# Kernel tuning notes

Hardware: AMD Instinct MI355X
Metric: run time of the kernel (lower is better)

## Reference

```python
import jax, jax.numpy as jnp
import numpy as np

E, N, D, H = 500000, 100000, 8, 256
BN_EPS = 1e-5


def _batchnorm(x, gamma, beta):
    # BatchNorm1d in training mode: biased batch statistics over dim 0
    mu = jnp.mean(x, axis=0)
    var = jnp.var(x, axis=0)
    return (x - mu) * jax.lax.rsqrt(var + BN_EPS) * gamma + beta


def _encoder(x, W1, b1, gamma, beta, W2, b2):
    h = jax.nn.relu(x @ W1 + b1)
    h = _batchnorm(h, gamma, beta)
    return h @ W2 + b2


def setup_inputs() -> dict:
    key = jax.random.key(0)
    ks = jax.random.split(key, 24)
    s = 0.05  # weight init scale
    inp = {
        "edge_attr": jax.random.normal(ks[0], (E, D), dtype=jnp.float32),
        "node_features": jax.random.normal(ks[1], (N, D), dtype=jnp.float32),
        "edge_index": jax.random.randint(ks[2], (2, E), 0, N, dtype=jnp.int32),
        "e_W1": jax.random.normal(ks[3], (D, H)) * s,
        "e_b1": jax.random.normal(ks[4], (H,)) * s,
        "e_gamma": jnp.ones((H,), jnp.float32),
        "e_beta": jnp.zeros((H,), jnp.float32),
        "e_W2": jax.random.normal(ks[5], (H, H)) * s,
        "e_b2": jax.random.normal(ks[6], (H,)) * s,
        "n_W1": jax.random.normal(ks[7], (D, H)) * s,
        "n_b1": jax.random.normal(ks[8], (H,)) * s,
        "n_gamma": jnp.ones((H,), jnp.float32),
        "n_beta": jnp.zeros((H,), jnp.float32),
        "n_W2": jax.random.normal(ks[9], (H, H)) * s,
        "n_b2": jax.random.normal(ks[10], (H,)) * s,
        "Wv": jax.random.normal(ks[11], (H, H)) * s,
        "bv": jax.random.normal(ks[12], (H,)) * s,
        "Wo": jax.random.normal(ks[13], (H, H)) * s,
        "bo": jax.random.normal(ks[14], (H,)) * s,
        "Wp": jax.random.normal(ks[15], (H, D)) * s,
        "bp": jax.random.normal(ks[16], (D,)) * s,
    }
    return inp


def reference(edge_attr, node_features, edge_index,
              e_W1, e_b1, e_gamma, e_beta, e_W2, e_b2,
              n_W1, n_b1, n_gamma, n_beta, n_W2, n_b2,
              Wv, bv, Wo, bo, Wp, bp):
    # edge encoder: Linear -> ReLU -> BatchNorm1d -> Linear
    edge_encoded = _encoder(edge_attr, e_W1, e_b1, e_gamma, e_beta, e_W2, e_b2)

    # gather endpoint features and average (node dim == edge dim, slice is no-op)
    src = node_features[edge_index[0]]  # [E, D]
    tgt = node_features[edge_index[1]]  # [E, D]
    node_context = (src + tgt) * 0.5
    node_encoded = _encoder(node_context, n_W1, n_b1, n_gamma, n_beta, n_W2, n_b2)

    # MultiheadAttention with seq_len=1: softmax over one key is exactly 1,
    # so output = out_proj(v_proj(node_encoded)); q/k projections cancel.
    attn_out = (node_encoded @ Wv + bv) @ Wo + bo  # [E, H]

    edge_attr_enhanced = attn_out @ Wp + bp  # [E, D]
    return edge_attr + 0.5 * edge_attr_enhanced
```

## Files before the change

kernel.cpp:

```cpp
#include <hip/hip_runtime.h>
#include <hip/hip_bf16.h>
#include <string.h>

#define E_CNT 500000
#define N_CNT 100000
#define HID   256
#define NTILE 31250

typedef short short8 __attribute__((ext_vector_type(8)));
typedef float f32x4 __attribute__((ext_vector_type(4)));

__device__ __forceinline__ unsigned short f2bf(float f){
  union { float f; unsigned int i; } v; v.f = f;
  unsigned int u = v.i;
  u = u + 0x7FFFu + ((u >> 16) & 1u);
  return (unsigned short)(u >> 16);
}

__device__ __forceinline__ unsigned int pk_bf16(float a, float b){
  __hip_bfloat162 p = __float22bfloat162_rn(make_float2(a, b));
  unsigned int u; memcpy(&u, &p, 4); return u;
}

__device__ __forceinline__ void init_w1_lds(unsigned short* w1l,
                                            const float* W1, const float* b1,
                                            int tid){
  int ch = tid;
  #pragma unroll
  for (int j = 0; j < 8; ++j){
    unsigned short w = f2bf(W1[j * HID + ch]);
    w1l[ch * 24 + j]     = w;
    w1l[ch * 24 + 8 + j] = w;
  }
  w1l[ch * 24 + 16] = f2bf(2.0f * b1[ch]);
  #pragma unroll
  for (int j = 17; j < 24; ++j) w1l[ch * 24 + j] = 0;
  if (tid < 32) w1l[256 * 24 + tid] = 0;
}

__global__ __launch_bounds__(256, 3) void k1_stats(
    const int* __restrict__ eidx, const float* __restrict__ nf,
    const float* __restrict__ W1, const float* __restrict__ b1,
    float* __restrict__ part, float* __restrict__ bd2)
{
  __shared__ unsigned short w1l[256 * 24 + 32];
  __shared__ unsigned short ctx[4][16 * 40];
  __shared__ float sred[2][4][128];

  const int tid = threadIdx.x, lane = tid & 63, wid = tid >> 6;
  const int cg = wid & 1;
  const int pair = (blockIdx.x * 4 + wid) >> 1;
  const int npair = gridDim.x * 2;
  const int m = lane & 15, q = lane >> 4;
  const int r = lane >> 2, side = (lane >> 1) & 1, half = lane & 1;

  if (blockIdx.x == 0 && tid < 16) bd2[tid] = 0.f;

  init_w1_lds(w1l, W1, b1, tid);

  unsigned short* myctx = ctx[wid];
  for (int i = lane; i < 16 * 40; i += 64) myctx[i] = 0;
  if (lane < 16) myctx[lane * 40 + 16] = 0x3F80;
  __syncthreads();

  short8 w1fr[8];
  #pragma unroll
  for (int nt = 0; nt < 8; ++nt)
    w1fr[nt] = *(const short8*)&w1l[((cg * 8 + nt) * 16 + m) * 24 + q * 8];

  const f32x4 z4 = {0.f, 0.f, 0.f, 0.f};
  f32x4 sacc[8], qacc[8];
  #pragma unroll
  for (int nt = 0; nt < 8; ++nt){ sacc[nt] = z4; qacc[nt] = z4; }

  int t = pair;
  float4 nfc = make_float4(0.f,0.f,0.f,0.f); int i1 = 0;
  if (t < NTILE){
    int id0 = eidx[side * E_CNT + t * 16 + r];
    nfc = ((const float4*)nf)[id0 * 2 + half];
  }
  { int tn = t + npair;
    if (tn < NTILE) i1 = eidx[side * E_CNT + tn * 16 + r]; }

  for (; t < NTILE; t += npair){
    *(uint2*)&myctx[r * 40 + side * 8 + half * 4] =
        make_uint2(pk_bf16(nfc.x, nfc.y), pk_bf16(nfc.z, nfc.w));

    int tn1 = t + npair, tn2 = t + 2 * npair;
    float4 nfn = make_float4(0.f,0.f,0.f,0.f); int i2 = 0;
    if (tn1 < NTILE) nfn = ((const float4*)nf)[i1 * 2 + half];
    if (tn2 < NTILE) i2 = eidx[side * E_CNT + tn2 * 16 + r];

    asm volatile("s_waitcnt lgkmcnt(0)" ::: "memory");
    short8 bfr = *(const short8*)&myctx[m * 40 + q * 8];
    #pragma unroll
    for (int nt = 0; nt < 8; ++nt){
      f32x4 c = __builtin_amdgcn_mfma_f32_16x16x32_bf16(w1fr[nt], bfr, z4, 0, 0, 0);
      f32x4 hv = __builtin_elementwise_max(c, z4);
      sacc[nt] += hv;
      qacc[nt] += hv * hv;
    }
    nfc = nfn; i1 = i2;
  }

  #pragma unroll
  for (int nt = 0; nt < 8; ++nt){
    #pragma unroll
    for (int i = 0; i < 4; ++i){
      float v = sacc[nt][i], w = qacc[nt][i];
      v += __shfl_xor(v, 1); w += __shfl_xor(w, 1);
      v += __shfl_xor(v, 2); w += __shfl_xor(w, 2);
      v += __shfl_xor(v, 4); w += __shfl_xor(w, 4);
      v += __shfl_xor(v, 8); w += __shfl_xor(w, 8);
      if (m == 0){
        int loc = nt * 16 + q * 4 + i;
        sred[0][wid][loc] = v;
        sred[1][wid][loc] = w;
      }
    }
  }
  __syncthreads();
  {
    int j = tid, hf = j >> 7, loc = j & 127;
    float s0 = sred[0][hf][loc] + sred[0][hf + 2][loc];
    float s1 = sred[1][hf][loc] + sred[1][hf + 2][loc];
    part[blockIdx.x * 512 + j]       = s0;
    part[blockIdx.x * 512 + 256 + j] = s1;
  }
}

__global__ __launch_bounds__(256) void kMid(
    const float* __restrict__ part, int nb,
    const float* __restrict__ gamma, const float* __restrict__ beta,
    const float* __restrict__ nW2,
    const float* __restrict__ Wv, const float* __restrict__ Wo,
    const float* __restrict__ Wp,
    const float* __restrict__ bv, const float* __restrict__ bo,
    const float* __restrict__ bp, const float* __restrict__ nb2,
    unsigned short* __restrict__ wd2t, float* __restrict__ bd2)
{
  __shared__ float WpL[2048];
  __shared__ float T1L[2048];
  __shared__ float T2L[2048];
  __shared__ float scr[2048];
  __shared__ float stL[8];
  const int t = threadIdx.x, b = blockIdx.x;

  for (int i = t; i < 2048; i += 256) WpL[i] = Wp[i];
  __syncthreads();

  {
    const float4* row = (const float4*)(Wo + t * HID);
    f32x4 a0 = {0.f,0.f,0.f,0.f}, a1 = {0.f,0.f,0.f,0.f};
    #pragma unroll 8
    for (int j4 = 0; j4 < 64; ++j4){
      float4 w = row[j4];
      const f32x4* xp = (const f32x4*)&WpL[j4 * 32];
      a0 += w.x * xp[0]; a1 += w.x * xp[1];
      a0 += w.y * xp[2]; a1 += w.y * xp[3];
      a0 += w.z * xp[4]; a1 += w.z * xp[5];
      a0 += w.w * xp[6]; a1 += w.w * xp[7];
    }
    *(f32x4*)&T1L[t * 8]     = a0;
    *(f32x4*)&T1L[t * 8 + 4] = a1;
  }
  __syncthreads();

  {
    const float4* row = (const float4*)(Wv + t * HID);
    f32x4 a0 = {0.f,0.f,0.f,0.f}, a1 = {0.f,0.f,0.f,0.f};
    #pragma unroll 8
    for (int j4 = 0; j4 < 64; ++j4){
      float4 w = row[j4];
      const f32x4* xp = (const f32x4*)&T1L[j4 * 32];
      a0 += w.x * xp[0]; a1 += w.x * xp[1];
      a0 += w.y * xp[2]; a1 += w.y * xp[3];
      a0 += w.z * xp[4]; a1 += w.z * xp[5];
      a0 += w.w * xp[6]; a1 += w.w * xp[7];
    }
    *(f32x4*)&T2L[t * 8]     = a0;
    *(f32x4*)&T2L[t * 8 + 4] = a1;
  }
  __syncthreads();

  {
    int cl = t >> 6, i = t & 63;
    int c = b * 4 + cl;
    float s0 = 0.f, s1 = 0.f;
    for (int b2 = i; b2 < nb; b2 += 64){
      s0 += part[b2 * 512 + c];
      s1 += part[b2 * 512 + 256 + c];
    }
    scr[cl * 128 + i]      = s0;
    scr[cl * 128 + 64 + i] = s1;
  }
  __syncthreads();
  if (t < 4){
    float s0 = 0.f, s1 = 0.f;
    for (int i = 0; i < 64; ++i){
      s0 += scr[t * 128 + i];
      s1 += scr[t * 128 + 64 + i];
    }
    const float invE = 1.0f / (float)E_CNT;
    float mu  = s0 * invE;
    float var = fmaxf(s1 * invE - mu * mu, 0.f);
    float s   = gamma[b * 4 + t] * rsqrtf(var + 4.0f * 1e-5f);
    stL[t]     = s;
    stL[4 + t] = beta[b * 4 + t] - mu * s;
  }
  __syncthreads();

  {
    int cl = t >> 6, d = (t >> 3) & 7, p8 = t & 7;
    int c = b * 4 + cl;
    const float* row = nW2 + c * HID;
    float a = 0.f;
    for (int j = p8 * 32; j < p8 * 32 + 32; ++j)
      a = fmaf(row[j], T2L[j * 8 + d], a);
    scr[t] = a;
  }
  __syncthreads();
  {
    int cl = t >> 6, d = (t >> 3) & 7, p8 = t & 7;
    if (p8 == 0){
      float w = 0.f;
      #pragma unroll
      for (int i = 0; i < 8; ++i) w += scr[t + i];
      int c = b * 4 + cl;
      wd2t[d * HID + c]       = f2bf(0.5f * stL[cl] * w);
      wd2t[(8 + d) * HID + c] = 0;
      scr[1024 + cl * 8 + d]  = stL[4 + cl] * w;
    }
  }
  __syncthreads();
  if (t < 8){
    float a = scr[1024 + t] + scr[1024 + 8 + t] +
              scr[1024 + 16 + t] + scr[1024 + 24 + t];
    #pragma unroll
    for (int jj = 0; jj < 4; ++jj){
      int j = 4 * b + jj;
      a = fmaf(nb2[j], T2L[j * 8 + t], a);
      a = fmaf(bv[j],  T1L[j * 8 + t], a);
      a = fmaf(bo[j],  WpL[j * 8 + t], a);
    }
    if (b == 0) a += bp[t];
    atomicAdd(&bd2[t], a);
  }
}

__global__ __launch_bounds__(256, 3) void k3_main(
    const int* __restrict__ eidx, const float* __restrict__ nf,
    const float* __restrict__ ea,
    const float* __restrict__ W1, const float* __restrict__ b1,
    const unsigned short* __restrict__ wd2t, const float* __restrict__ bd2,
    float* __restrict__ out)
{
  __shared__ unsigned short w1l[256 * 24 + 32];
  __shared__ unsigned short ctx[4][16 * 40];
  __shared__ unsigned short hbuf[4][16 * 264];

  const int tid = threadIdx.x, lane = tid & 63, wid = tid >> 6;
  const int gw = blockIdx.x * 4 + wid, ngw = gridDim.x * 4;
  const int m = lane & 15, q = lane >> 4;
  const int r = lane >> 2, side = (lane >> 1) & 1, half = lane & 1;

  init_w1_lds(w1l, W1, b1, tid);

  short8 w2fr[8];
  #pragma unroll
  for (int kb = 0; kb < 8; ++kb)
    w2fr[kb] = *(const short8*)&wd2t[m * HID + kb * 32 + q * 8];
  const float bd2v = (m < 8) ? 0.5f * bd2[m] : 0.f;

  unsigned short* myctx = ctx[wid];
  unsigned short* myh   = hbuf[wid];
  for (int i = lane; i < 16 * 40; i += 64) myctx[i] = 0;
  if (lane < 16) myctx[lane * 40 + 16] = 0x3F80;
  __syncthreads();

  short8 w1fr[16];
  #pragma unroll
  for (int nt = 0; nt < 16; ++nt)
    w1fr[nt] = *(const short8*)&w1l[(nt * 16 + m) * 24 + q * 8];

  const f32x4 z4 = {0.f, 0.f, 0.f, 0.f};

  int t = gw;
  float4 nfc = make_float4(0.f,0.f,0.f,0.f); int i1 = 0;
  if (t < NTILE){
    int id0 = eidx[side * E_CNT + t * 16 + r];
    nfc = ((const float4*)nf)[id0 * 2 + half];
  }
  { int tn = t + ngw;
    if (tn < NTILE) i1 = eidx[side * E_CNT + tn * 16 + r]; }

  const bool dok = (m < 8);
  for (; t < NTILE; t += ngw){
    *(uint2*)&myctx[r * 40 + side * 8 + half * 4] =
        make_uint2(pk_bf16(nfc.x, nfc.y), pk_bf16(nfc.z, nfc.w));

    float eav[4];
    #pragma unroll
    for (int i = 0; i < 4; ++i)
      eav[i] = dok ? ea[(t * 16 + q * 4 + i) * 8 + m] : 0.f;

    int tn1 = t + ngw, tn2 = t + 2 * ngw;
    float4 nfn = make_float4(0.f,0.f,0.f,0.f); int i2 = 0;
    if (tn1 < NTILE) nfn = ((const float4*)nf)[i1 * 2 + half];
    if (tn2 < NTILE) i2 = eidx[side * E_CNT + tn2 * 16 + r];

    asm volatile("s_waitcnt lgkmcnt(0)" ::: "memory");
    short8 bfr = *(const short8*)&myctx[m * 40 + q * 8];
    #pragma unroll
    for (int nt = 0; nt < 16; ++nt){
      f32x4 c = __builtin_amdgcn_mfma_f32_16x16x32_bf16(w1fr[nt], bfr, z4, 0, 0, 0);
      f32x4 hv = __builtin_elementwise_max(c, z4);
      *(uint2*)&myh[m * 264 + nt * 16 + q * 4] =
          make_uint2(pk_bf16(hv[0], hv[1]), pk_bf16(hv[2], hv[3]));
    }
    asm volatile("s_waitcnt lgkmcnt(0)" ::: "memory");
    f32x4 acc = z4;
    #pragma unroll
    for (int kb = 0; kb < 8; ++kb){
      short8 afr = *(const short8*)&myh[m * 264 + kb * 32 + q * 8];
      acc = __builtin_amdgcn_mfma_f32_16x16x32_bf16(afr, w2fr[kb], acc, 0, 0, 0);
    }
    if (dok){
      #pragma unroll
      for (int i = 0; i < 4; ++i){
        float o = eav[i] + acc[i] + bd2v;
        out[(t * 16 + q * 4 + i) * 8 + m] = o;
      }
    }
    nfc = nfn; i1 = i2;
  }
}

extern "C" void kernel_launch(void* const* d_in, const int* in_sizes, int n_in,
                              void* d_out, int out_size, void* d_ws, size_t ws_size,
                              hipStream_t stream)
{
  const float* ea   = (const float*)d_in[0];
  const float* nf   = (const float*)d_in[1];
  const int*   eidx = (const int*)d_in[2];
  const float* nW1    = (const float*)d_in[9];
  const float* nb1    = (const float*)d_in[10];
  const float* ngamma = (const float*)d_in[11];
  const float* nbeta  = (const float*)d_in[12];
  const float* nW2    = (const float*)d_in[13];
  const float* nb2    = (const float*)d_in[14];
  const float* Wv     = (const float*)d_in[15];
  const float* bv     = (const float*)d_in[16];
  const float* Wo     = (const float*)d_in[17];
  const float* bo     = (const float*)d_in[18];
  const float* Wp     = (const float*)d_in[19];
  const float* bp     = (const float*)d_in[20];

  long avail = (long)ws_size - 8192 - 64 - 16384;
  int nb = (int)(avail / 2048);
  if (nb > 768) nb = 768;
  if (nb < 1)   nb = 1;

  char* ws = (char*)d_ws;
  size_t off = (size_t)nb * 2048;
  float* ws_part          = (float*)(ws + 0);
  unsigned short* ws_wd2t = (unsigned short*)(ws + off);
  float* ws_bd2           = (float*)(ws + off + 8192);

  k1_stats<<<dim3(nb), dim3(256), 0, stream>>>(eidx, nf, nW1, nb1,
                                               ws_part, ws_bd2);
  kMid<<<dim3(64), dim3(256), 0, stream>>>(
      ws_part, nb, ngamma, nbeta, nW2, Wv, Wo, Wp, bv, bo, bp, nb2,
      ws_wd2t, ws_bd2);
  k3_main<<<dim3(768), dim3(256), 0, stream>>>(
      eidx, nf, ea, nW1, nb1, ws_wd2t, ws_bd2, (float*)d_out);
}
```

Before: 199.0 us.

## Materialize gathered bf16 node context in stats kernel and reuse it in main kernel

```diff
diff --git a/kernel.cpp b/kernel.cpp
--- a/kernel.cpp
+++ b/kernel.cpp
@@ -41,7 +41,8 @@
 __global__ __launch_bounds__(256, 3) void k1_stats(
     const int* __restrict__ eidx, const float* __restrict__ nf,
     const float* __restrict__ W1, const float* __restrict__ b1,
-    float* __restrict__ part, float* __restrict__ bd2)
+    float* __restrict__ part, float* __restrict__ bd2,
+    unsigned short* __restrict__ ctxw)
 {
   __shared__ unsigned short w1l[256 * 24 + 32];
   __shared__ unsigned short ctx[4][16 * 40];
@@ -83,8 +84,10 @@
     if (tn < NTILE) i1 = eidx[side * E_CNT + tn * 16 + r]; }
 
   for (; t < NTILE; t += npair){
-    *(uint2*)&myctx[r * 40 + side * 8 + half * 4] =
-        make_uint2(pk_bf16(nfc.x, nfc.y), pk_bf16(nfc.z, nfc.w));
+    uint2 pkd = make_uint2(pk_bf16(nfc.x, nfc.y), pk_bf16(nfc.z, nfc.w));
+    *(uint2*)&myctx[r * 40 + side * 8 + half * 4] = pkd;
+    if (cg == 0)
+      *(uint2*)&ctxw[(size_t)t * 256 + r * 16 + side * 8 + half * 4] = pkd;
 
     int tn1 = t + npair, tn2 = t + 2 * npair;
     float4 nfn = make_float4(0.f,0.f,0.f,0.f); int i2 = 0;
@@ -249,20 +252,18 @@
 }
 
 __global__ __launch_bounds__(256, 3) void k3_main(
-    const int* __restrict__ eidx, const float* __restrict__ nf,
     const float* __restrict__ ea,
     const float* __restrict__ W1, const float* __restrict__ b1,
     const unsigned short* __restrict__ wd2t, const float* __restrict__ bd2,
+    const unsigned short* __restrict__ ctxw,
     float* __restrict__ out)
 {
   __shared__ unsigned short w1l[256 * 24 + 32];
-  __shared__ unsigned short ctx[4][16 * 40];
   __shared__ unsigned short hbuf[4][16 * 264];
 
   const int tid = threadIdx.x, lane = tid & 63, wid = tid >> 6;
   const int gw = blockIdx.x * 4 + wid, ngw = gridDim.x * 4;
   const int m = lane & 15, q = lane >> 4;
-  const int r = lane >> 2, side = (lane >> 1) & 1, half = lane & 1;
 
   init_w1_lds(w1l, W1, b1, tid);
 
@@ -272,10 +273,7 @@
     w2fr[kb] = *(const short8*)&wd2t[m * HID + kb * 32 + q * 8];
   const float bd2v = (m < 8) ? 0.5f * bd2[m] : 0.f;
 
-  unsigned short* myctx = ctx[wid];
-  unsigned short* myh   = hbuf[wid];
-  for (int i = lane; i < 16 * 40; i += 64) myctx[i] = 0;
-  if (lane < 16) myctx[lane * 40 + 16] = 0x3F80;
+  unsigned short* myh = hbuf[wid];
   __syncthreads();
 
   short8 w1fr[16];
@@ -285,35 +283,30 @@
 
   const f32x4 z4 = {0.f, 0.f, 0.f, 0.f};
 
+  short8 kc = {0,0,0,0,0,0,0,0};
+  if (q == 2) kc[0] = (short)0x3F80;
+  const bool ld  = (q < 2);
+  const bool dok = (m < 8);
+
   int t = gw;
-  float4 nfc = make_float4(0.f,0.f,0.f,0.f); int i1 = 0;
-  if (t < NTILE){
-    int id0 = eidx[side * E_CNT + t * 16 + r];
-    nfc = ((const float4*)nf)[id0 * 2 + half];
-  }
-  { int tn = t + ngw;
-    if (tn < NTILE) i1 = eidx[side * E_CNT + tn * 16 + r]; }
-
-  const bool dok = (m < 8);
+  short8 bcur = kc;
+  if (ld && t < NTILE)
+    bcur = *(const short8*)&ctxw[(size_t)t * 256 + m * 16 + q * 8];
+
   for (; t < NTILE; t += ngw){
-    *(uint2*)&myctx[r * 40 + side * 8 + half * 4] =
-        make_uint2(pk_bf16(nfc.x, nfc.y), pk_bf16(nfc.z, nfc.w));
+    int tn = t + ngw;
+    short8 bnext = kc;
+    if (ld && tn < NTILE)
+      bnext = *(const short8*)&ctxw[(size_t)tn * 256 + m * 16 + q * 8];
 
     float eav[4];
     #pragma unroll
     for (int i = 0; i < 4; ++i)
       eav[i] = dok ? ea[(t * 16 + q * 4 + i) * 8 + m] : 0.f;
 
-    int tn1 = t + ngw, tn2 = t + 2 * ngw;
-    float4 nfn = make_float4(0.f,0.f,0.f,0.f); int i2 = 0;
-    if (tn1 < NTILE) nfn = ((const float4*)nf)[i1 * 2 + half];
-    if (tn2 < NTILE) i2 = eidx[side * E_CNT + tn2 * 16 + r];
-
-    asm volatile("s_waitcnt lgkmcnt(0)" ::: "memory");
-    short8 bfr = *(const short8*)&myctx[m * 40 + q * 8];
     #pragma unroll
     for (int nt = 0; nt < 16; ++nt){
-      f32x4 c = __builtin_amdgcn_mfma_f32_16x16x32_bf16(w1fr[nt], bfr, z4, 0, 0, 0);
+      f32x4 c = __builtin_amdgcn_mfma_f32_16x16x32_bf16(w1fr[nt], bcur, z4, 0, 0, 0);
       f32x4 hv = __builtin_elementwise_max(c, z4);
       *(uint2*)&myh[m * 264 + nt * 16 + q * 4] =
           make_uint2(pk_bf16(hv[0], hv[1]), pk_bf16(hv[2], hv[3]));
@@ -332,7 +325,7 @@
         out[(t * 16 + q * 4 + i) * 8 + m] = o;
       }
     }
-    nfc = nfn; i1 = i2;
+    bcur = bnext;
   }
 }
 
@@ -356,7 +349,8 @@
   const float* Wp     = (const float*)d_in[19];
   const float* bp     = (const float*)d_in[20];
 
-  long avail = (long)ws_size - 8192 - 64 - 16384;
+  const size_t CTX_BYTES = (size_t)NTILE * 512;
+  long avail = (long)ws_size - 8192 - 64 - (long)CTX_BYTES - 1024;
   int nb = (int)(avail / 2048);
   if (nb > 768) nb = 768;
   if (nb < 1)   nb = 1;
@@ -366,12 +360,13 @@
   float* ws_part          = (float*)(ws + 0);
   unsigned short* ws_wd2t = (unsigned short*)(ws + off);
   float* ws_bd2           = (float*)(ws + off + 8192);
+  unsigned short* ws_ctx  = (unsigned short*)(ws + off + 8192 + 64);
 
   k1_stats<<<dim3(nb), dim3(256), 0, stream>>>(eidx, nf, nW1, nb1,
-                                               ws_part, ws_bd2);
+                                               ws_part, ws_bd2, ws_ctx);
   kMid<<<dim3(64), dim3(256), 0, stream>>>(
       ws_part, nb, ngamma, nbeta, nW2, Wv, Wo, Wp, bv, bo, bp, nb2,
       ws_wd2t, ws_bd2);
   k3_main<<<dim3(768), dim3(256), 0, stream>>>(
-      eidx, nf, ea, nW1, nb1, ws_wd2t, ws_bd2, (float*)d_out);
-}
+      ea, nW1, nb1, ws_wd2t, ws_bd2, ws_ctx, (float*)d_out);
+}
```

New measurement: 198.8 us. No clear change (-0.1%).
